# Optimization experiments

Measured on AMD Instinct MI355X. Metric: run time of the kernel, lower is better.

## Reference

```python
import jax, jax.numpy as jnp
import numpy as np

B, S, D, H = 1, 4096, 1024, 16
HD = D // H  # head_dim = 64


def setup_inputs() -> dict:
    key = jax.random.key(0)
    k1, k2, k3 = jax.random.split(key, 3)
    scale = 0.02
    return {
        "x": jax.random.normal(k1, (B, S, D), dtype=jnp.float32),
        "w_qkv": jax.random.normal(k2, (D, 3 * D), dtype=jnp.float32) * scale,
        "b_qkv": jnp.zeros((3 * D,), dtype=jnp.float32),
        "w_proj": jax.random.normal(k3, (D, D), dtype=jnp.float32) * scale,
        "b_proj": jnp.zeros((D,), dtype=jnp.float32),
    }


def reference(x, w_qkv, b_qkv, w_proj, b_proj):
    b, s, d = x.shape
    qkv = x @ w_qkv + b_qkv                      # [b, s, 3d]
    q, k, v = jnp.split(qkv, 3, axis=-1)
    # [b, h, s, hd]
    q = q.reshape(b, s, H, HD).transpose(0, 2, 1, 3)
    k = k.reshape(b, s, H, HD).transpose(0, 2, 1, 3)
    v = v.reshape(b, s, H, HD).transpose(0, 2, 1, 3)
    score = jnp.einsum("bhqd,bhkd->bhqk", q, k) / jnp.sqrt(jnp.float32(HD))
    causal = jnp.tril(jnp.ones((s, s), dtype=bool))
    score = jnp.where(causal, score, -jnp.inf)
    attn = jax.nn.softmax(score, axis=-1)        # dropout omitted (eval mode, p effectively 0)
    out = jnp.einsum("bhqk,bhkd->bhqd", attn, v)  # [b, h, s, hd]
    out = out.transpose(0, 2, 1, 3).reshape(b, s, d)
    return out @ w_proj + b_proj
```

## Files before the change

kernel.cpp:

```cpp
#include <hip/hip_runtime.h>
#include <hip/hip_bf16.h>
#include <math.h>

typedef __bf16 bf16;
typedef __bf16 bf16x8 __attribute__((ext_vector_type(8)));
typedef __bf16 bf16x4 __attribute__((ext_vector_type(4)));
typedef float f32x4 __attribute__((ext_vector_type(4)));

#define S_ 4096
#define D_ 1024
#define H_ 16
#define HD_ 64
#define N3_ 3072
#define NSPLIT 2

typedef const __attribute__((address_space(1))) void* gas1_t;
typedef __attribute__((address_space(3))) void* las3_t;
static __device__ __forceinline__ void g2l16(const void* g, void* l) {
  __builtin_amdgcn_global_load_lds((gas1_t)g, (las3_t)l, 16, 0, 0);
}

__global__ __launch_bounds__(256) void prep_kernel(const float* __restrict__ x,
                                                   bf16* __restrict__ xb,
                                                   const float* __restrict__ w_qkv,
                                                   bf16* __restrict__ wqkvT,
                                                   const float* __restrict__ w_proj,
                                                   bf16* __restrict__ wprojT) {
  __shared__ float t[32][33];
  const int b = blockIdx.x;
  if (b < 4096) {
    int i = (b * 256 + threadIdx.x) * 4;
    float4 v = *(const float4*)(x + i);
    bf16x4 o;
    o.x = (bf16)v.x; o.y = (bf16)v.y; o.z = (bf16)v.z; o.w = (bf16)v.w;
    *(bf16x4*)(xb + i) = o;
    return;
  }
  const float* in; bf16* outp; int ldin, bx, by;
  if (b < 7168) { int b2 = b - 4096; in = w_qkv;  outp = wqkvT;  ldin = N3_; bx = (b2 % 96) * 32; by = (b2 / 96) * 32; }
  else          { int b3 = b - 7168; in = w_proj; outp = wprojT; ldin = D_;  bx = (b3 % 32) * 32; by = (b3 / 32) * 32; }
  const int tx = threadIdx.x & 31, ty = threadIdx.x >> 5;
#pragma unroll
  for (int i = 0; i < 4; ++i)
    t[ty + i * 8][tx] = in[(size_t)(by + ty + i * 8) * ldin + bx + tx];
  __syncthreads();
#pragma unroll
  for (int i = 0; i < 4; ++i)
    outp[(size_t)(bx + ty + i * 8) * D_ + by + tx] = (bf16)t[tx][ty + i * 8];
}

template <int BN>
__global__ __launch_bounds__(256) void gemm_bt(const bf16* __restrict__ A,
                                               const bf16* __restrict__ Bt,
                                               const float* __restrict__ bias,
                                               bf16* __restrict__ outb,
                                               float* __restrict__ outf,
                                               bf16* __restrict__ vTout,
                                               int M, int N, int K,
                                               int qlim, float qscale) {
  constexpr int NT = BN / 32;
  __shared__ bf16 sA[128 * 32];
  __shared__ bf16 sB[BN * 32];
  const int tid = threadIdx.x;
  const int wave = tid >> 6, lane = tid & 63;
  const int col = lane & 15, quad = lane >> 4;
  const int wm = (wave & 1) * 64, wn = (wave >> 1) * (BN / 2);
  const long bm = (long)blockIdx.x * 128, bn = (long)blockIdx.y * BN;
  const int srow = tid >> 2;
  const int soff = (tid & 3) * 8;

  f32x4 acc[4][NT] = {};

  for (int kb = 0; kb < K; kb += 32) {
    __syncthreads();
    g2l16(A + (bm + srow) * (long)K + kb + soff,      &sA[tid * 8]);
    g2l16(A + (bm + 64 + srow) * (long)K + kb + soff, &sA[2048 + tid * 8]);
#pragma unroll
    for (int i = 0; i < BN / 64; ++i)
      g2l16(Bt + (bn + i * 64 + srow) * (long)K + kb + soff, &sB[i * 2048 + tid * 8]);
    __syncthreads();

    bf16x8 af[4], bfr[NT];
#pragma unroll
    for (int t = 0; t < 4; ++t)
      af[t] = *(const bf16x8*)(&sA[(wm + t * 16 + col) * 32 + quad * 8]);
#pragma unroll
    for (int t = 0; t < NT; ++t)
      bfr[t] = *(const bf16x8*)(&sB[(wn + t * 16 + col) * 32 + quad * 8]);
#pragma unroll
    for (int mt = 0; mt < 4; ++mt)
#pragma unroll
      for (int nt = 0; nt < NT; ++nt)
        acc[mt][nt] = __builtin_amdgcn_mfma_f32_16x16x32_bf16(af[mt], bfr[nt], acc[mt][nt], 0, 0, 0);
  }

#pragma unroll
  for (int mt = 0; mt < 4; ++mt) {
#pragma unroll
    for (int nt = 0; nt < NT; ++nt) {
      long gn = bn + wn + nt * 16 + col;
      float bv = bias ? bias[gn] : 0.f;
      if (vTout && gn >= 2 * D_) {
        bf16x4 vv;
        long gm0 = bm + wm + mt * 16 + quad * 4;
#pragma unroll
        for (int i = 0; i < 4; ++i) vv[i] = (bf16)(acc[mt][nt][i] + bv);
        *(bf16x4*)(&vTout[(gn - 2 * D_) * (long)S_ + gm0]) = vv;
      } else {
        float sc = (gn < qlim) ? qscale : 1.0f;
#pragma unroll
        for (int i = 0; i < 4; ++i) {
          long gm = bm + wm + mt * 16 + quad * 4 + i;
          float v = (acc[mt][nt][i] + bv) * sc;
          if (outf) outf[gm * N + gn] = v;
          else      outb[gm * N + gn] = (bf16)v;
        }
      }
    }
  }
}

__global__ __launch_bounds__(512, 2) void gemm256_qkv(const bf16* __restrict__ A,
                                                      const bf16* __restrict__ Bt,
                                                      const float* __restrict__ bias,
                                                      bf16* __restrict__ outb,
                                                      bf16* __restrict__ vTout,
                                                      float qscale) {
  __shared__ bf16 smem[65536];
  const int K = D_;
  const int NTK = K / 64;
  const int tid = threadIdx.x;
  const int lane = tid & 63, wv = tid >> 6;
  const int col = lane & 15, quad = lane >> 4;
  const int wr = wv >> 2, wc = wv & 3;
  const long bm = (long)blockIdx.x * 256, bn = (long)blockIdx.y * 256;

  int srowA[2][2], srowB[2][2];
  int schA[2][2], schB[2][2];
#pragma unroll
  for (int q = 0; q < 2; ++q) {
    int slot = q * 512 + tid;
    int rl = slot >> 3, ch = slot & 7;
#pragma unroll
    for (int h = 0; h < 2; ++h) {
      int rowA = (rl & 63) | (h << 6) | ((rl >> 6) << 7);
      srowA[h][q] = rowA; schA[h][q] = ch ^ (rowA & 7);
      int rowB = (rl & 31) | (h << 5) | ((rl >> 5) << 6);
      srowB[h][q] = rowB; schB[h][q] = ch ^ (rowB & 7);
    }
  }
  const int dstoff = tid * 8;

  const int ck[2] = { ((0 * 4 + quad) ^ (col & 7)) * 8, ((1 * 4 + quad) ^ (col & 7)) * 8 };

#define STAGE_A(h, T, buf)                                                        \
  {                                                                               \
    const int kbs = (T) * 64;                                                     \
    bf16* lb = smem + (buf) * 32768 + (h) * 8192;                                 \
    g2l16(A + (bm + srowA[h][0]) * (long)K + kbs + schA[h][0] * 8, lb + dstoff);  \
    g2l16(A + (bm + srowA[h][1]) * (long)K + kbs + schA[h][1] * 8, lb + 4096 + dstoff); \
  }
#define STAGE_B(h, T, buf)                                                        \
  {                                                                               \
    const int kbs = (T) * 64;                                                     \
    bf16* lb = smem + (buf) * 32768 + 16384 + (h) * 8192;                         \
    g2l16(Bt + (bn + srowB[h][0]) * (long)K + kbs + schB[h][0] * 8, lb + dstoff); \
    g2l16(Bt + (bn + srowB[h][1]) * (long)K + kbs + schB[h][1] * 8, lb + 4096 + dstoff); \
  }

  f32x4 acc[8][4] = {};

  STAGE_A(0, 0, 0);
  STAGE_A(1, 0, 0);
  STAGE_B(0, 0, 0);
  STAGE_A(0, 1, 1);
  STAGE_B(1, 0, 0);

  for (int G = 0; G < NTK; ++G) {
    const int cur = G & 1;
    const bf16* bufc = smem + cur * 32768;
    const bool last = (G == NTK - 1);

    bf16x8 afr[4][2], bfr[2][2][2];

    if (last) asm volatile("s_waitcnt vmcnt(2)" ::: "memory");
    else      asm volatile("s_waitcnt vmcnt(4)" ::: "memory");
    __builtin_amdgcn_s_barrier();
    __builtin_amdgcn_sched_barrier(0);
#pragma unroll
    for (int mt = 0; mt < 4; ++mt) {
      const bf16* rp = bufc + (wr * 64 + mt * 16 + col) * 64;
      afr[mt][0] = *(const bf16x8*)(rp + ck[0]);
      afr[mt][1] = *(const bf16x8*)(rp + ck[1]);
    }
#pragma unroll
    for (int nt = 0; nt < 2; ++nt) {
      const bf16* rp = bufc + 16384 + (wc * 32 + nt * 16 + col) * 64;
      bfr[0][nt][0] = *(const bf16x8*)(rp + ck[0]);
      bfr[0][nt][1] = *(const bf16x8*)(rp + ck[1]);
    }
    if (G + 1 < NTK) STAGE_A(1, G + 1, cur ^ 1);
    asm volatile("s_waitcnt lgkmcnt(0)" ::: "memory");
    __builtin_amdgcn_sched_barrier(0);
    __builtin_amdgcn_s_setprio(1);
#pragma unroll
    for (int mt = 0; mt < 4; ++mt)
#pragma unroll
      for (int nt = 0; nt < 2; ++nt) {
        acc[mt][nt] = __builtin_amdgcn_mfma_f32_16x16x32_bf16(afr[mt][0], bfr[0][nt][0], acc[mt][nt], 0, 0, 0);
        acc[mt][nt] = __builtin_amdgcn_mfma_f32_16x16x32_bf16(afr[mt][1], bfr[0][nt][1], acc[mt][nt], 0, 0, 0);
      }
    __builtin_amdgcn_s_setprio(0);

    if (last) asm volatile("s_waitcnt vmcnt(0)" ::: "memory");
    else      asm volatile("s_waitcnt vmcnt(2)" ::: "memory");
    __builtin_amdgcn_s_barrier();
    __builtin_amdgcn_sched_barrier(0);
#pragma unroll
    for (int nt = 0; nt < 2; ++nt) {
      const bf16* rp = bufc + 16384 + 8192 + (wc * 32 + nt * 16 + col) * 64;
      bfr[1][nt][0] = *(const bf16x8*)(rp + ck[0]);
      bfr[1][nt][1] = *(const bf16x8*)(rp + ck[1]);
    }
    if (G + 1 < NTK) STAGE_B(0, G + 1, cur ^ 1);
    asm volatile("s_waitcnt lgkmcnt(0)" ::: "memory");
    __builtin_amdgcn_sched_barrier(0);
    __builtin_amdgcn_s_setprio(1);
#pragma unroll
    for (int mt = 0; mt < 4; ++mt)
#pragma unroll
      for (int nt = 0; nt < 2; ++nt) {
        acc[mt][2 + nt] = __builtin_amdgcn_mfma_f32_16x16x32_bf16(afr[mt][0], bfr[1][nt][0], acc[mt][2 + nt], 0, 0, 0);
        acc[mt][2 + nt] = __builtin_amdgcn_mfma_f32_16x16x32_bf16(afr[mt][1], bfr[1][nt][1], acc[mt][2 + nt], 0, 0, 0);
      }
    __builtin_amdgcn_s_setprio(0);

    __builtin_amdgcn_s_barrier();
    __builtin_amdgcn_sched_barrier(0);
#pragma unroll
    for (int mt = 0; mt < 4; ++mt) {
      const bf16* rp = bufc + 8192 + (wr * 64 + mt * 16 + col) * 64;
      afr[mt][0] = *(const bf16x8*)(rp + ck[0]);
      afr[mt][1] = *(const bf16x8*)(rp + ck[1]);
    }
    if (G + 2 < NTK) STAGE_A(0, G + 2, cur);
    asm volatile("s_waitcnt lgkmcnt(0)" ::: "memory");
    __builtin_amdgcn_sched_barrier(0);
    __builtin_amdgcn_s_setprio(1);
#pragma unroll
    for (int mt = 0; mt < 4; ++mt)
#pragma unroll
      for (int nt = 0; nt < 2; ++nt) {
        acc[4 + mt][2 + nt] = __builtin_amdgcn_mfma_f32_16x16x32_bf16(afr[mt][0], bfr[1][nt][0], acc[4 + mt][2 + nt], 0, 0, 0);
        acc[4 + mt][2 + nt] = __builtin_amdgcn_mfma_f32_16x16x32_bf16(afr[mt][1], bfr[1][nt][1], acc[4 + mt][2 + nt], 0, 0, 0);
      }
    __builtin_amdgcn_s_setprio(0);

    __builtin_amdgcn_s_barrier();
    __builtin_amdgcn_sched_barrier(0);
    if (G + 1 < NTK) STAGE_B(1, G + 1, cur ^ 1);
    __builtin_amdgcn_s_setprio(1);
#pragma unroll
    for (int mt = 0; mt < 4; ++mt)
#pragma unroll
      for (int nt = 0; nt < 2; ++nt) {
        acc[4 + mt][nt] = __builtin_amdgcn_mfma_f32_16x16x32_bf16(afr[mt][0], bfr[0][nt][0], acc[4 + mt][nt], 0, 0, 0);
        acc[4 + mt][nt] = __builtin_amdgcn_mfma_f32_16x16x32_bf16(afr[mt][1], bfr[0][nt][1], acc[4 + mt][nt], 0, 0, 0);
      }
    __builtin_amdgcn_s_setprio(0);
  }

  const bool isV = (blockIdx.y >= 8);
  const bool isQ = (blockIdx.y < 4);
#pragma unroll
  for (int mh = 0; mh < 2; ++mh)
#pragma unroll
    for (int mt = 0; mt < 4; ++mt)
#pragma unroll
      for (int nh = 0; nh < 2; ++nh)
#pragma unroll
        for (int nt = 0; nt < 2; ++nt) {
          long gn = bn + wc * 64 + nh * 32 + nt * 16 + col;
          float bv = bias[gn];
          long gm0 = bm + wr * 128 + mh * 64 + mt * 16 + quad * 4;
          f32x4 a = acc[mh * 4 + mt][nh * 2 + nt];
          if (isV) {
            bf16x4 vv;
#pragma unroll
            for (int i = 0; i < 4; ++i) vv[i] = (bf16)(a[i] + bv);
            *(bf16x4*)(&vTout[(gn - 2 * D_) * (long)S_ + gm0]) = vv;
          } else {
            float sc = isQ ? qscale : 1.0f;
#pragma unroll
            for (int i = 0; i < 4; ++i)
              outb[(gm0 + i) * (long)N3_ + gn] = (bf16)((a[i] + bv) * sc);
          }
        }
#undef STAGE_A
#undef STAGE_B
}

__device__ __forceinline__ int swz_g(int row) {
  return (row & 3) | ((((row >> 2) ^ (row >> 3)) & 1) << 2);
}

__global__ __launch_bounds__(256) void attn_kernel(const bf16* __restrict__ qkv,
                                                   const bf16* __restrict__ vT,
                                                   bf16* __restrict__ Opart,
                                                   float* __restrict__ lws) {
  __shared__ bf16 sK[2][64 * 64];
  __shared__ bf16 sV[2][64 * 64];
  const int hh = blockIdx.x;
  const int qb = (int)(gridDim.y - 1 - blockIdx.y);
  const int sp = blockIdx.z;
  const int tid = threadIdx.x;
  const int wave = tid >> 6, lane = tid & 63;
  const int col = lane & 15, quad = lane >> 4;
  const int qbase = qb * 128 + wave * 32;

  const bf16* qp0 = qkv + (size_t)(qbase + col) * N3_ + hh * HD_;
  bf16x8 aq[2][2];
  aq[0][0] = *(const bf16x8*)(qp0 + quad * 8);
  aq[0][1] = *(const bf16x8*)(qp0 + 32 + quad * 8);
  aq[1][0] = *(const bf16x8*)(qp0 + 16 * N3_ + quad * 8);
  aq[1][1] = *(const bf16x8*)(qp0 + 16 * N3_ + 32 + quad * 8);

  bf16x8 ones;
#pragma unroll
  for (int j = 0; j < 8; ++j) ones[j] = (bf16)1.0f;

  f32x4 acc[2][4] = {};
  f32x4 acc_l[2] = {};

  const bf16* kgbase = qkv + D_ + hh * HD_;
  const bf16* vgbase = vT + (size_t)hh * HD_ * S_;
  const int krow = (col >> 2) * 8 + (col & 3);
  const int niter = 2 * (qb + 1);
  const int base = niter / NSPLIT, rem = niter % NSPLIT;
  const int it0 = sp * base + (sp < rem ? sp : rem);
  const int len = base + (sp < rem ? 1 : 0);
  const int it1 = it0 + len;

  const int srow = tid >> 2;
  const int sc0 = (tid & 3) * 2;
  const int gs = swz_g(srow);
  const int soff0 = srow * 64 + ((sc0 ^ gs) * 8);
  const int soff1 = srow * 64 + (((sc0 + 1) ^ gs) * 8);

  if (len > 0) {
    {
      const bf16* kg = kgbase + (size_t)(it0 * 64 + srow) * N3_ + sc0 * 8;
      const bf16* vg = vgbase + (size_t)srow * S_ + it0 * 64 + sc0 * 8;
      *(int4*)(&sK[0][soff0]) = *(const int4*)kg;
      *(int4*)(&sK[0][soff1]) = *(const int4*)(kg + 8);
      *(int4*)(&sV[0][soff0]) = *(const int4*)vg;
      *(int4*)(&sV[0][soff1]) = *(const int4*)(vg + 8);
    }
    __syncthreads();

    for (int j = it0; j < it1; ++j) {
      const int kb = j * 64;
      const int cur = (j - it0) & 1;
      const bool more = (j + 1 < it1);
      int4 pk0, pk1, pv0, pv1;
      if (more) {
        const bf16* kg = kgbase + (size_t)(kb + 64 + srow) * N3_ + sc0 * 8;
        const bf16* vg = vgbase + (size_t)srow * S_ + kb + 64 + sc0 * 8;
        pk0 = *(const int4*)kg; pk1 = *(const int4*)(kg + 8);
        pv0 = *(const int4*)vg; pv1 = *(const int4*)(vg + 8);
      }

      if (kb < qbase + 32) {
        const bool act0 = kb < qbase + 16;
        const bf16* kc = &sK[cur][0];
        const bf16* vc = &sV[cur][0];

        f32x4 st[2][4];
#pragma unroll
        for (int t = 0; t < 4; ++t) {
          int row = (t >> 1) * 32 + (t & 1) * 4 + krow;
          int pc = quad ^ swz_g(row);
          bf16x8 bk0 = *(const bf16x8*)(kc + row * 64 + pc * 8);
          bf16x8 bk1 = *(const bf16x8*)(kc + row * 64 + (pc ^ 4) * 8);
          if (act0) {
            f32x4 z = {};
            z = __builtin_amdgcn_mfma_f32_16x16x32_bf16(bk0, aq[0][0], z, 0, 0, 0);
            st[0][t] = __builtin_amdgcn_mfma_f32_16x16x32_bf16(bk1, aq[0][1], z, 0, 0, 0);
          }
          f32x4 z = {};
          z = __builtin_amdgcn_mfma_f32_16x16x32_bf16(bk0, aq[1][0], z, 0, 0, 0);
          st[1][t] = __builtin_amdgcn_mfma_f32_16x16x32_bf16(bk1, aq[1][1], z, 0, 0, 0);
        }

        bf16x8 pfrag[2][2];
#pragma unroll
        for (int s2 = 0; s2 < 2; ++s2) {
          if (s2 == 0 && !act0) continue;
          const int rowbase = qbase + 16 * s2;
          float p[4][4];
          if (kb + 63 <= rowbase) {
#pragma unroll
            for (int t = 0; t < 4; ++t)
#pragma unroll
              for (int r = 0; r < 4; ++r)
                p[t][r] = __builtin_amdgcn_exp2f(st[s2][t][r]);
          } else {
#pragma unroll
            for (int t = 0; t < 4; ++t)
#pragma unroll
              for (int r = 0; r < 4; ++r) {
                int key = kb + (t >> 1) * 32 + quad * 8 + (t & 1) * 4 + r;
                p[t][r] = (key > rowbase + col)
                              ? 0.f
                              : __builtin_amdgcn_exp2f(st[s2][t][r]);
              }
          }
#pragma unroll
          for (int c = 0; c < 2; ++c)
#pragma unroll
            for (int j2 = 0; j2 < 4; ++j2) {
              pfrag[s2][c][j2]     = (bf16)p[2 * c][j2];
              pfrag[s2][c][j2 + 4] = (bf16)p[2 * c + 1][j2];
            }
        }

#pragma unroll
        for (int c = 0; c < 2; ++c) {
#pragma unroll
          for (int n = 0; n < 4; ++n) {
            int row = n * 16 + col;
            int pc = (4 * c + quad) ^ swz_g(row);
            bf16x8 bv = *(const bf16x8*)(vc + row * 64 + pc * 8);
            if (act0)
              acc[0][n] = __builtin_amdgcn_mfma_f32_16x16x32_bf16(pfrag[0][c], bv, acc[0][n], 0, 0, 0);
            acc[1][n] = __builtin_amdgcn_mfma_f32_16x16x32_bf16(pfrag[1][c], bv, acc[1][n], 0, 0, 0);
          }
          if (act0)
            acc_l[0] = __builtin_amdgcn_mfma_f32_16x16x32_bf16(pfrag[0][c], ones, acc_l[0], 0, 0, 0);
          acc_l[1] = __builtin_amdgcn_mfma_f32_16x16x32_bf16(pfrag[1][c], ones, acc_l[1], 0, 0, 0);
        }
      }

      if (more) {
        bf16* kn = &sK[cur ^ 1][0];
        bf16* vn = &sV[cur ^ 1][0];
        *(int4*)(kn + soff0) = pk0;
        *(int4*)(kn + soff1) = pk1;
        *(int4*)(vn + soff0) = pv0;
        *(int4*)(vn + soff1) = pv1;
      }
      __syncthreads();
    }
  }

  bf16* Op = Opart + (size_t)sp * S_ * D_;
#pragma unroll
  for (int s2 = 0; s2 < 2; ++s2) {
    const int rowbase = qbase + 16 * s2;
    if (col == 0) {
#pragma unroll
      for (int r = 0; r < 4; ++r)
        lws[((size_t)sp * H_ + hh) * S_ + rowbase + quad * 4 + r] = acc_l[s2][r];
    }
#pragma unroll
    for (int n = 0; n < 4; ++n)
#pragma unroll
      for (int r = 0; r < 4; ++r)
        Op[(size_t)(rowbase + quad * 4 + r) * D_ + hh * HD_ + n * 16 + col] =
            (bf16)acc[s2][n][r];
  }
}

__global__ __launch_bounds__(256) void attn_combine(const bf16* __restrict__ Opart,
                                                    const float* __restrict__ lws,
                                                    bf16* __restrict__ outb) {
  int e = (blockIdx.x * 256 + threadIdx.x) * 8;
  int s = e >> 10;
  int h = (e & (D_ - 1)) >> 6;
  float l = 0.f;
#pragma unroll
  for (int sp = 0; sp < NSPLIT; ++sp) l += lws[((size_t)sp * H_ + h) * S_ + s];
  float inv = 1.0f / l;
  float o[8] = {};
#pragma unroll
  for (int sp = 0; sp < NSPLIT; ++sp) {
    bf16x8 a = *(const bf16x8*)(Opart + (size_t)sp * S_ * D_ + e);
#pragma unroll
    for (int j = 0; j < 8; ++j) o[j] += (float)a[j];
  }
  bf16x8 r;
#pragma unroll
  for (int j = 0; j < 8; ++j) r[j] = (bf16)(o[j] * inv);
  *(bf16x8*)(outb + e) = r;
}

extern "C" void kernel_launch(void* const* d_in, const int* in_sizes, int n_in,
                              void* d_out, int out_size, void* d_ws, size_t ws_size,
                              hipStream_t stream) {
  const float* x      = (const float*)d_in[0];
  const float* w_qkv  = (const float*)d_in[1];
  const float* b_qkv  = (const float*)d_in[2];
  const float* w_proj = (const float*)d_in[3];
  const float* b_proj = (const float*)d_in[4];
  float* out = (float*)d_out;

  bf16* xb     = (bf16*)d_ws;
  bf16* wqkvT  = xb + (size_t)S_ * D_;
  bf16* wprojT = wqkvT + (size_t)N3_ * D_;
  bf16* qkv    = wprojT + (size_t)D_ * D_;
  bf16* vT     = qkv + (size_t)S_ * N3_;
  bf16* Opart  = vT + (size_t)D_ * S_;
  float* lws   = (float*)(Opart + (size_t)NSPLIT * S_ * D_);
  bf16* attn   = xb;

  const float QSCALE = 0.125f * 1.44269504088896f;

  prep_kernel<<<dim3(8192), 256, 0, stream>>>(x, xb, w_qkv, wqkvT, w_proj, wprojT);
  gemm256_qkv<<<dim3(S_ / 256, N3_ / 256), 512, 0, stream>>>(
      xb, wqkvT, b_qkv, qkv, vT, QSCALE);
  attn_kernel<<<dim3(H_, S_ / 128, NSPLIT), 256, 0, stream>>>(qkv, vT, Opart, lws);
  attn_combine<<<dim3((S_ * D_) / 2048), 256, 0, stream>>>(Opart, lws, attn);
  gemm_bt<128><<<dim3(S_ / 128, D_ / 128), 256, 0, stream>>>(
      attn, wprojT, b_proj, nullptr, out, nullptr, S_, D_, D_, 0, 1.0f);
}
```

Baseline: 206.6 us.

## Process two KV chunks per barrier with quad-buffered LDS; shrink proj GEMM tile

The attention loop now handles two 64-key chunks per iteration and keeps four LDS buffers. It prefetches the next two chunks into registers and then writes them to the idle pair, which halves the number of __syncthreads calls and gives more independent MFMA work between barriers. Because niter is always even, the split is simplified to equal halves. The output projection GEMM now uses a 64-wide N tile, doubling its grid. In exchange, LDS use doubles and register pressure rises, which may reduce occupancy.

```diff
diff --git a/kernel.cpp b/kernel.cpp
--- a/kernel.cpp
+++ b/kernel.cpp
@@ -308,8 +308,8 @@
                                                    const bf16* __restrict__ vT,
                                                    bf16* __restrict__ Opart,
                                                    float* __restrict__ lws) {
-  __shared__ bf16 sK[2][64 * 64];
-  __shared__ bf16 sV[2][64 * 64];
+  __shared__ bf16 sK[4][64 * 64];
+  __shared__ bf16 sV[4][64 * 64];
   const int hh = blockIdx.x;
   const int qb = (int)(gridDim.y - 1 - blockIdx.y);
   const int sp = blockIdx.z;
@@ -336,9 +336,8 @@
   const bf16* vgbase = vT + (size_t)hh * HD_ * S_;
   const int krow = (col >> 2) * 8 + (col & 3);
   const int niter = 2 * (qb + 1);
-  const int base = niter / NSPLIT, rem = niter % NSPLIT;
-  const int it0 = sp * base + (sp < rem ? sp : rem);
-  const int len = base + (sp < rem ? 1 : 0);
+  const int len = niter / NSPLIT;
+  const int it0 = sp * len;
   const int it1 = it0 + len;
 
   const int srow = tid >> 2;
@@ -347,111 +346,136 @@
   const int soff0 = srow * 64 + ((sc0 ^ gs) * 8);
   const int soff1 = srow * 64 + (((sc0 + 1) ^ gs) * 8);
 
-  if (len > 0) {
+  {
+    const bf16* kg = kgbase + (size_t)(it0 * 64 + srow) * N3_ + sc0 * 8;
+    const bf16* vg = vgbase + (size_t)srow * S_ + it0 * 64 + sc0 * 8;
+    *(int4*)(&sK[0][soff0]) = *(const int4*)kg;
+    *(int4*)(&sK[0][soff1]) = *(const int4*)(kg + 8);
+    *(int4*)(&sV[0][soff0]) = *(const int4*)vg;
+    *(int4*)(&sV[0][soff1]) = *(const int4*)(vg + 8);
+    if (it0 + 1 < it1) {
+      const bf16* kg1 = kg + (size_t)64 * N3_;
+      const bf16* vg1 = vg + 64;
+      *(int4*)(&sK[1][soff0]) = *(const int4*)kg1;
+      *(int4*)(&sK[1][soff1]) = *(const int4*)(kg1 + 8);
+      *(int4*)(&sV[1][soff0]) = *(const int4*)vg1;
+      *(int4*)(&sV[1][soff1]) = *(const int4*)(vg1 + 8);
+    }
+  }
+  __syncthreads();
+
+#define CHUNK_BODY(KB, BI)                                                        \
+  if ((KB) < qbase + 32) {                                                        \
+    const bool act0 = (KB) < qbase + 16;                                          \
+    const bf16* kc = &sK[BI][0];                                                  \
+    const bf16* vc = &sV[BI][0];                                                  \
+    f32x4 st[2][4];                                                               \
+    _Pragma("unroll")                                                             \
+    for (int t = 0; t < 4; ++t) {                                                 \
+      int row = (t >> 1) * 32 + (t & 1) * 4 + krow;                               \
+      int pc = quad ^ swz_g(row);                                                 \
+      bf16x8 kf0 = *(const bf16x8*)(kc + row * 64 + pc * 8);                      \
+      bf16x8 kf1 = *(const bf16x8*)(kc + row * 64 + (pc ^ 4) * 8);                \
+      if (act0) {                                                                 \
+        f32x4 z = {};                                                             \
+        z = __builtin_amdgcn_mfma_f32_16x16x32_bf16(kf0, aq[0][0], z, 0, 0, 0);   \
+        st[0][t] = __builtin_amdgcn_mfma_f32_16x16x32_bf16(kf1, aq[0][1], z, 0, 0, 0); \
+      }                                                                           \
+      f32x4 z = {};                                                               \
+      z = __builtin_amdgcn_mfma_f32_16x16x32_bf16(kf0, aq[1][0], z, 0, 0, 0);     \
+      st[1][t] = __builtin_amdgcn_mfma_f32_16x16x32_bf16(kf1, aq[1][1], z, 0, 0, 0); \
+    }                                                                             \
+    bf16x8 pfrag[2][2];                                                           \
+    _Pragma("unroll")                                                             \
+    for (int s2 = 0; s2 < 2; ++s2) {                                              \
+      if (s2 == 0 && !act0) continue;                                             \
+      const int rowbase = qbase + 16 * s2;                                        \
+      float p[4][4];                                                              \
+      if ((KB) + 63 <= rowbase) {                                                 \
+        _Pragma("unroll")                                                         \
+        for (int t = 0; t < 4; ++t)                                               \
+          _Pragma("unroll")                                                       \
+          for (int r = 0; r < 4; ++r)                                             \
+            p[t][r] = __builtin_amdgcn_exp2f(st[s2][t][r]);                       \
+      } else {                                                                    \
+        _Pragma("unroll")                                                         \
+        for (int t = 0; t < 4; ++t)                                               \
+          _Pragma("unroll")                                                       \
+          for (int r = 0; r < 4; ++r) {                                           \
+            int key = (KB) + (t >> 1) * 32 + quad * 8 + (t & 1) * 4 + r;          \
+            p[t][r] = (key > rowbase + col) ? 0.f                                 \
+                                            : __builtin_amdgcn_exp2f(st[s2][t][r]); \
+          }                                                                       \
+      }                                                                           \
+      _Pragma("unroll")                                                           \
+      for (int c = 0; c < 2; ++c)                                                 \
+        _Pragma("unroll")                                                         \
+        for (int j2 = 0; j2 < 4; ++j2) {                                          \
+          pfrag[s2][c][j2]     = (bf16)p[2 * c][j2];                              \
+          pfrag[s2][c][j2 + 4] = (bf16)p[2 * c + 1][j2];                          \
+        }                                                                         \
+    }                                                                             \
+    _Pragma("unroll")                                                             \
+    for (int c = 0; c < 2; ++c) {                                                 \
+      _Pragma("unroll")                                                           \
+      for (int n = 0; n < 4; ++n) {                                               \
+        int row = n * 16 + col;                                                   \
+        int pc = (4 * c + quad) ^ swz_g(row);                                     \
+        bf16x8 vf = *(const bf16x8*)(vc + row * 64 + pc * 8);                     \
+        if (act0)                                                                 \
+          acc[0][n] = __builtin_amdgcn_mfma_f32_16x16x32_bf16(pfrag[0][c], vf, acc[0][n], 0, 0, 0); \
+        acc[1][n] = __builtin_amdgcn_mfma_f32_16x16x32_bf16(pfrag[1][c], vf, acc[1][n], 0, 0, 0);   \
+      }                                                                           \
+      if (act0)                                                                   \
+        acc_l[0] = __builtin_amdgcn_mfma_f32_16x16x32_bf16(pfrag[0][c], ones, acc_l[0], 0, 0, 0);   \
+      acc_l[1] = __builtin_amdgcn_mfma_f32_16x16x32_bf16(pfrag[1][c], ones, acc_l[1], 0, 0, 0);     \
+    }                                                                             \
+  }
+
+  for (int j0 = it0; j0 < it1; j0 += 2) {
+    const int bb = (((j0 - it0) >> 1) & 1) * 2;
+    const bool hasB = (j0 + 1 < it1);
+    const bool pfA = (j0 + 2 < it1);
+    const bool pfB = (j0 + 3 < it1);
+
+    int4 nk00, nk01, nv00, nv01, nk10, nk11, nv10, nv11;
+    if (pfA) {
+      const bf16* kg = kgbase + (size_t)((j0 + 2) * 64 + srow) * N3_ + sc0 * 8;
+      const bf16* vg = vgbase + (size_t)srow * S_ + (j0 + 2) * 64 + sc0 * 8;
+      nk00 = *(const int4*)kg; nk01 = *(const int4*)(kg + 8);
+      nv00 = *(const int4*)vg; nv01 = *(const int4*)(vg + 8);
+    }
+    if (pfB) {
+      const bf16* kg = kgbase + (size_t)((j0 + 3) * 64 + srow) * N3_ + sc0 * 8;
+      const bf16* vg = vgbase + (size_t)srow * S_ + (j0 + 3) * 64 + sc0 * 8;
+      nk10 = *(const int4*)kg; nk11 = *(const int4*)(kg + 8);
+      nv10 = *(const int4*)vg; nv11 = *(const int4*)(vg + 8);
+    }
+
     {
-      const bf16* kg = kgbase + (size_t)(it0 * 64 + srow) * N3_ + sc0 * 8;
-      const bf16* vg = vgbase + (size_t)srow * S_ + it0 * 64 + sc0 * 8;
-      *(int4*)(&sK[0][soff0]) = *(const int4*)kg;
-      *(int4*)(&sK[0][soff1]) = *(const int4*)(kg + 8);
-      *(int4*)(&sV[0][soff0]) = *(const int4*)vg;
-      *(int4*)(&sV[0][soff1]) = *(const int4*)(vg + 8);
+      const int kb0 = j0 * 64;
+      CHUNK_BODY(kb0, bb);
+    }
+    if (hasB) {
+      const int kb1 = (j0 + 1) * 64;
+      CHUNK_BODY(kb1, bb + 1);
+    }
+
+    if (pfA) {
+      bf16* kn = &sK[bb ^ 2][0];
+      bf16* vn = &sV[bb ^ 2][0];
+      *(int4*)(kn + soff0) = nk00; *(int4*)(kn + soff1) = nk01;
+      *(int4*)(vn + soff0) = nv00; *(int4*)(vn + soff1) = nv01;
+    }
+    if (pfB) {
+      bf16* kn = &sK[(bb ^ 2) + 1][0];
+      bf16* vn = &sV[(bb ^ 2) + 1][0];
+      *(int4*)(kn + soff0) = nk10; *(int4*)(kn + soff1) = nk11;
+      *(int4*)(vn + soff0) = nv10; *(int4*)(vn + soff1) = nv11;
     }
     __syncthreads();
-
-    for (int j = it0; j < it1; ++j) {
-      const int kb = j * 64;
-      const int cur = (j - it0) & 1;
-      const bool more = (j + 1 < it1);
-      int4 pk0, pk1, pv0, pv1;
-      if (more) {
-        const bf16* kg = kgbase + (size_t)(kb + 64 + srow) * N3_ + sc0 * 8;
-        const bf16* vg = vgbase + (size_t)srow * S_ + kb + 64 + sc0 * 8;
-        pk0 = *(const int4*)kg; pk1 = *(const int4*)(kg + 8);
-        pv0 = *(const int4*)vg; pv1 = *(const int4*)(vg + 8);
-      }
-
-      if (kb < qbase + 32) {
-        const bool act0 = kb < qbase + 16;
-        const bf16* kc = &sK[cur][0];
-        const bf16* vc = &sV[cur][0];
-
-        f32x4 st[2][4];
-#pragma unroll
-        for (int t = 0; t < 4; ++t) {
-          int row = (t >> 1) * 32 + (t & 1) * 4 + krow;
-          int pc = quad ^ swz_g(row);
-          bf16x8 bk0 = *(const bf16x8*)(kc + row * 64 + pc * 8);
-          bf16x8 bk1 = *(const bf16x8*)(kc + row * 64 + (pc ^ 4) * 8);
-          if (act0) {
-            f32x4 z = {};
-            z = __builtin_amdgcn_mfma_f32_16x16x32_bf16(bk0, aq[0][0], z, 0, 0, 0);
-            st[0][t] = __builtin_amdgcn_mfma_f32_16x16x32_bf16(bk1, aq[0][1], z, 0, 0, 0);
-          }
-          f32x4 z = {};
-          z = __builtin_amdgcn_mfma_f32_16x16x32_bf16(bk0, aq[1][0], z, 0, 0, 0);
-          st[1][t] = __builtin_amdgcn_mfma_f32_16x16x32_bf16(bk1, aq[1][1], z, 0, 0, 0);
-        }
-
-        bf16x8 pfrag[2][2];
-#pragma unroll
-        for (int s2 = 0; s2 < 2; ++s2) {
-          if (s2 == 0 && !act0) continue;
-          const int rowbase = qbase + 16 * s2;
-          float p[4][4];
-          if (kb + 63 <= rowbase) {
-#pragma unroll
-            for (int t = 0; t < 4; ++t)
-#pragma unroll
-              for (int r = 0; r < 4; ++r)
-                p[t][r] = __builtin_amdgcn_exp2f(st[s2][t][r]);
-          } else {
-#pragma unroll
-            for (int t = 0; t < 4; ++t)
-#pragma unroll
-              for (int r = 0; r < 4; ++r) {
-                int key = kb + (t >> 1) * 32 + quad * 8 + (t & 1) * 4 + r;
-                p[t][r] = (key > rowbase + col)
-                              ? 0.f
-                              : __builtin_amdgcn_exp2f(st[s2][t][r]);
-              }
-          }
-#pragma unroll
-          for (int c = 0; c < 2; ++c)
-#pragma unroll
-            for (int j2 = 0; j2 < 4; ++j2) {
-              pfrag[s2][c][j2]     = (bf16)p[2 * c][j2];
-              pfrag[s2][c][j2 + 4] = (bf16)p[2 * c + 1][j2];
-            }
-        }
-
-#pragma unroll
-        for (int c = 0; c < 2; ++c) {
-#pragma unroll
-          for (int n = 0; n < 4; ++n) {
-            int row = n * 16 + col;
-            int pc = (4 * c + quad) ^ swz_g(row);
-            bf16x8 bv = *(const bf16x8*)(vc + row * 64 + pc * 8);
-            if (act0)
-              acc[0][n] = __builtin_amdgcn_mfma_f32_16x16x32_bf16(pfrag[0][c], bv, acc[0][n], 0, 0, 0);
-            acc[1][n] = __builtin_amdgcn_mfma_f32_16x16x32_bf16(pfrag[1][c], bv, acc[1][n], 0, 0, 0);
-          }
-          if (act0)
-            acc_l[0] = __builtin_amdgcn_mfma_f32_16x16x32_bf16(pfrag[0][c], ones, acc_l[0], 0, 0, 0);
-          acc_l[1] = __builtin_amdgcn_mfma_f32_16x16x32_bf16(pfrag[1][c], ones, acc_l[1], 0, 0, 0);
-        }
-      }
-
-      if (more) {
-        bf16* kn = &sK[cur ^ 1][0];
-        bf16* vn = &sV[cur ^ 1][0];
-        *(int4*)(kn + soff0) = pk0;
-        *(int4*)(kn + soff1) = pk1;
-        *(int4*)(vn + soff0) = pv0;
-        *(int4*)(vn + soff1) = pv1;
-      }
-      __syncthreads();
-    }
-  }
+  }
+#undef CHUNK_BODY
 
   bf16* Op = Opart + (size_t)sp * S_ * D_;
 #pragma unroll
@@ -520,6 +544,6 @@
       xb, wqkvT, b_qkv, qkv, vT, QSCALE);
   attn_kernel<<<dim3(H_, S_ / 128, NSPLIT), 256, 0, stream>>>(qkv, vT, Opart, lws);
   attn_combine<<<dim3((S_ * D_) / 2048), 256, 0, stream>>>(Opart, lws, attn);
-  gemm_bt<128><<<dim3(S_ / 128, D_ / 128), 256, 0, stream>>>(
+  gemm_bt<64><<<dim3(S_ / 128, D_ / 64), 256, 0, stream>>>(
       attn, wprojT, b_proj, nullptr, out, nullptr, S_, D_, D_, 0, 1.0f);
 }
```

Result: faster. 195.3 us (-5.5%).
